# Kernel tuning notes

Measured on AMD Instinct MI355X. Metric: run time of the kernel, lower is better.

## Reference

```python
import jax, jax.numpy as jnp
import numpy as np

N = 50000   # nodes
E = 600000  # edges
D = 128     # node_features (EvolveGCNO in=out channels)
H = 128     # hidden_dim (final Linear out)


def setup_inputs() -> dict:
    key = jax.random.key(0)
    ks = jax.random.split(key, 9)
    stdv = 1.0 / np.sqrt(D)
    u = lambda k, shape: jax.random.uniform(k, shape, jnp.float32, -stdv, stdv)
    return {
        "x": jax.random.normal(ks[0], (N, D), jnp.float32),
        "edge_index": jax.random.randint(ks[1], (2, E), 0, N),
        "edge_weight": jax.random.uniform(ks[2], (E,), jnp.float32),
        "W0": u(ks[3], (D, D)),        # EvolveGCNO initial_weight (squeezed)
        "w_ih": u(ks[4], (3 * D, D)),  # GRU input weights (r|z|n)
        "w_hh": u(ks[5], (3 * D, D)),  # GRU hidden weights (r|z|n)
        "b_ih": u(ks[6], (3 * D,)),
        "b_hh": u(ks[7], (3 * D,)),
        "W_lin": u(ks[8], (H, D)),     # torch Linear weight [out, in]
        "b_lin": jnp.zeros((H,), jnp.float32),
    }


def _gru_step(x, h, w_ih, w_hh, b_ih, b_hh):
    # One torch.nn.GRU cell step; here x == h == W0 (weight evolution).
    gi = x @ w_ih.T + b_ih
    gh = h @ w_hh.T + b_hh
    i_r, i_z, i_n = jnp.split(gi, 3, axis=-1)
    h_r, h_z, h_n = jnp.split(gh, 3, axis=-1)
    r = jax.nn.sigmoid(i_r + h_r)
    z = jax.nn.sigmoid(i_z + h_z)
    n = jnp.tanh(i_n + r * h_n)
    return (1.0 - z) * n + z * h


def reference(x, edge_index, edge_weight, W0, w_ih, w_hh, b_ih, b_hh, W_lin, b_lin):
    # 1) Evolve the GCN weight with one GRU step (input = hidden = W0).
    W = _gru_step(W0, W0, w_ih, w_hh, b_ih, b_hh)  # [D, D]

    # 2) GCNConv_Fixed_W: add self-loops (weight 1), symmetric normalization.
    loops = jnp.arange(N)
    row = jnp.concatenate([edge_index[0], loops])  # source
    col = jnp.concatenate([edge_index[1], loops])  # target
    ew = jnp.concatenate([edge_weight, jnp.ones((N,), x.dtype)])
    deg = jax.ops.segment_sum(ew, col, num_segments=N)
    dinv = jnp.where(deg > 0, jax.lax.rsqrt(deg), 0.0)
    norm = dinv[row] * ew * dinv[col]  # [E+N]

    xw = x @ W                                        # [N, D]
    h = jax.ops.segment_sum(norm[:, None] * xw[row], col, num_segments=N)  # [N, D]

    # 3) ReLU + Linear
    h = jax.nn.relu(h)
    return h @ W_lin.T + b_lin  # [N, H]
```

## Files before the change

### kernel.cpp

```cpp
#include <hip/hip_runtime.h>
#include <hip/hip_bf16.h>

#define NN 50000
#define EE 600000
#define DD 128
#define CAP 48
#define CNT_SHIFT 25
#define SUM_MASK 0x1FFFFFFu

typedef __attribute__((ext_vector_type(8))) __bf16 bf16x8;
typedef __attribute__((ext_vector_type(8))) short short8;
typedef __attribute__((ext_vector_type(4))) float f32x4;

__device__ __forceinline__ unsigned short f2bf(float f) {
    union { float f; unsigned u; } c; c.f = f;
    unsigned r = (c.u + 0x7fffu + ((c.u >> 16) & 1u)) >> 16;
    return (unsigned short)r;
}
__device__ __forceinline__ float bflo(unsigned u) {
    union { unsigned u; float f; } c; c.u = u << 16; return c.f;
}
__device__ __forceinline__ float bfhi(unsigned u) {
    union { unsigned u; float f; } c; c.u = u & 0xffff0000u; return c.f;
}
__device__ __forceinline__ float degof(unsigned p) {
    return 1.0f + (float)(p & SUM_MASK) * (1.0f / 65536.0f);
}

__global__ __launch_bounds__(256) void init_kernel(
    unsigned* __restrict__ cnt32,
    const float* __restrict__ W0, const float* __restrict__ w_ih,
    const float* __restrict__ w_hh, const float* __restrict__ b_ih,
    const float* __restrict__ b_hh, unsigned short* __restrict__ Wbt,
    const float* __restrict__ x, short* __restrict__ xb)
{
    if (blockIdx.x >= 113) {
        int u = (blockIdx.x - 113) * 256 + threadIdx.x;
        if (u < NN * DD / 8) {
            const float4* p = (const float4*)x + (size_t)u * 2;
            float4 f0 = p[0], f1 = p[1];
            short8 v;
            v[0] = (short)f2bf(f0.x); v[1] = (short)f2bf(f0.y);
            v[2] = (short)f2bf(f0.z); v[3] = (short)f2bf(f0.w);
            v[4] = (short)f2bf(f1.x); v[5] = (short)f2bf(f1.y);
            v[6] = (short)f2bf(f1.z); v[7] = (short)f2bf(f1.w);
            *(short8*)(xb + (size_t)u * 8) = v;
        }
        return;
    }
    if (blockIdx.x < 49) {
        int i = blockIdx.x * 256 + threadIdx.x;
        if (i < 50176 * 4 / 16) ((uint4*)cnt32)[i] = make_uint4(0u, 0u, 0u, 0u);
        return;
    }
    int idx = (blockIdx.x - 49) * 256 + threadIdx.x;
    int i = idx >> 7, j = idx & 127;
    const float4* a  = (const float4*)(W0  + i * DD);
    const float4* pr = (const float4*)(w_ih + (j        ) * DD);
    const float4* pz = (const float4*)(w_ih + (j + 128  ) * DD);
    const float4* pn = (const float4*)(w_ih + (j + 256  ) * DD);
    const float4* qr = (const float4*)(w_hh + (j        ) * DD);
    const float4* qz = (const float4*)(w_hh + (j + 128  ) * DD);
    const float4* qn = (const float4*)(w_hh + (j + 256  ) * DD);
    float ir = 0.f, iz = 0.f, inn = 0.f, hr = 0.f, hz = 0.f, hn = 0.f;
    for (int d = 0; d < DD / 4; ++d) {
        float4 av = a[d];
        float4 t;
        t = pr[d]; ir  += av.x*t.x + av.y*t.y + av.z*t.z + av.w*t.w;
        t = pz[d]; iz  += av.x*t.x + av.y*t.y + av.z*t.z + av.w*t.w;
        t = pn[d]; inn += av.x*t.x + av.y*t.y + av.z*t.z + av.w*t.w;
        t = qr[d]; hr  += av.x*t.x + av.y*t.y + av.z*t.z + av.w*t.w;
        t = qz[d]; hz  += av.x*t.x + av.y*t.y + av.z*t.z + av.w*t.w;
        t = qn[d]; hn  += av.x*t.x + av.y*t.y + av.z*t.z + av.w*t.w;
    }
    ir += b_ih[j]; iz += b_ih[j + 128]; inn += b_ih[j + 256];
    hr += b_hh[j]; hz += b_hh[j + 128]; hn  += b_hh[j + 256];
    float r = 1.f / (1.f + expf(-(ir + hr)));
    float z = 1.f / (1.f + expf(-(iz + hz)));
    float n = tanhf(inn + r * hn);
    float w = (1.f - z) * n + z * W0[idx];
    Wbt[j * DD + i] = f2bf(w);
}

__global__ __launch_bounds__(256) void histfill_kernel(
    const int* __restrict__ row, const int* __restrict__ col,
    const float* __restrict__ ew,
    unsigned* __restrict__ cnt32, unsigned* __restrict__ edges)
{
    int e = blockIdx.x * 512 + threadIdx.x;
#pragma unroll
    for (int q = 0; q < 2; ++q, e += 256) {
        if (e < EE) {
            int c = col[e];
            unsigned wq = (unsigned)(ew[e] * 65536.0f);
            if (wq > 65535u) wq = 65535u;
            unsigned old = atomicAdd(&cnt32[c], (1u << CNT_SHIFT) | wq);
            unsigned oldcnt = old >> CNT_SHIFT;
            if (oldcnt < CAP)
                edges[(size_t)c * CAP + oldcnt] = (unsigned)row[e] | (wq << 16);
        }
    }
}

__global__ __launch_bounds__(256) void gather_kernel(
    const unsigned* __restrict__ edges, const unsigned* __restrict__ cnt32,
    const unsigned* __restrict__ xbu, unsigned* __restrict__ aggu)
{
    int wid  = threadIdx.x >> 6;
    int lane = threadIdx.x & 63;
    int base = (blockIdx.x * 4 + wid) * 2;
    if (base >= NN) return;
    bool hasB = (base + 1) < NN;

    unsigned pnA = cnt32[base];
    unsigned pnB = hasB ? cnt32[base + 1] : 0u;
    int nA = (int)(pnA >> CNT_SHIFT); if (nA > CAP) nA = CAP;
    int nB = hasB ? (int)(pnB >> CNT_SHIFT) : 0; if (nB > CAP) nB = CAP;
    const unsigned* ebA = edges + (size_t)base * CAP;
    const unsigned* ebB = edges + (size_t)(base + 1) * CAP;
    float sclA = rsqrtf(degof(pnA));
    float sclB = hasB ? rsqrtf(degof(pnB)) : 0.f;
    unsigned xsA = xbu[(size_t)base * 64 + lane];
    unsigned xsB = hasB ? xbu[(size_t)(base + 1) * 64 + lane] : 0u;
    float axA = sclA * bflo(xsA), ayA = sclA * bfhi(xsA);
    float axB = sclB * bflo(xsB), ayB = sclB * bfhi(xsB);

    int kA = 0, kB = 0;
    int nA4 = nA & ~3, nB4 = nB & ~3;
    while (kA < nA4 || kB < nB4) {
        if (kA < nA4) {
            uint4 rc = *(const uint4*)(ebA + kA);
            int s0 = (int)(rc.x & 0xFFFFu), s1 = (int)(rc.y & 0xFFFFu);
            int s2 = (int)(rc.z & 0xFFFFu), s3 = (int)(rc.w & 0xFFFFu);
            unsigned p0 = cnt32[s0], p1 = cnt32[s1], p2 = cnt32[s2], p3 = cnt32[s3];
            unsigned x0 = xbu[(size_t)s0 * 64 + lane];
            unsigned x1 = xbu[(size_t)s1 * 64 + lane];
            unsigned x2 = xbu[(size_t)s2 * 64 + lane];
            unsigned x3 = xbu[(size_t)s3 * 64 + lane];
            float v0 = (float)(rc.x >> 16) * (1.0f / 65536.0f) * rsqrtf(degof(p0));
            float v1 = (float)(rc.y >> 16) * (1.0f / 65536.0f) * rsqrtf(degof(p1));
            float v2 = (float)(rc.z >> 16) * (1.0f / 65536.0f) * rsqrtf(degof(p2));
            float v3 = (float)(rc.w >> 16) * (1.0f / 65536.0f) * rsqrtf(degof(p3));
            axA += v0 * bflo(x0) + v1 * bflo(x1) + v2 * bflo(x2) + v3 * bflo(x3);
            ayA += v0 * bfhi(x0) + v1 * bfhi(x1) + v2 * bfhi(x2) + v3 * bfhi(x3);
            kA += 4;
        }
        if (kB < nB4) {
            uint4 rc = *(const uint4*)(ebB + kB);
            int s0 = (int)(rc.x & 0xFFFFu), s1 = (int)(rc.y & 0xFFFFu);
            int s2 = (int)(rc.z & 0xFFFFu), s3 = (int)(rc.w & 0xFFFFu);
            unsigned p0 = cnt32[s0], p1 = cnt32[s1], p2 = cnt32[s2], p3 = cnt32[s3];
            unsigned x0 = xbu[(size_t)s0 * 64 + lane];
            unsigned x1 = xbu[(size_t)s1 * 64 + lane];
            unsigned x2 = xbu[(size_t)s2 * 64 + lane];
            unsigned x3 = xbu[(size_t)s3 * 64 + lane];
            float v0 = (float)(rc.x >> 16) * (1.0f / 65536.0f) * rsqrtf(degof(p0));
            float v1 = (float)(rc.y >> 16) * (1.0f / 65536.0f) * rsqrtf(degof(p1));
            float v2 = (float)(rc.z >> 16) * (1.0f / 65536.0f) * rsqrtf(degof(p2));
            float v3 = (float)(rc.w >> 16) * (1.0f / 65536.0f) * rsqrtf(degof(p3));
            axB += v0 * bflo(x0) + v1 * bflo(x1) + v2 * bflo(x2) + v3 * bflo(x3);
            ayB += v0 * bfhi(x0) + v1 * bfhi(x1) + v2 * bfhi(x2) + v3 * bfhi(x3);
            kB += 4;
        }
    }
    for (; kA < nA; ++kA) {
        unsigned r0 = ebA[kA];
        int s0 = (int)(r0 & 0xFFFFu);
        unsigned p0 = cnt32[s0];
        unsigned x0 = xbu[(size_t)s0 * 64 + lane];
        float v0 = (float)(r0 >> 16) * (1.0f / 65536.0f) * rsqrtf(degof(p0));
        axA += v0 * bflo(x0); ayA += v0 * bfhi(x0);
    }
    for (; kB < nB; ++kB) {
        unsigned r0 = ebB[kB];
        int s0 = (int)(r0 & 0xFFFFu);
        unsigned p0 = cnt32[s0];
        unsigned x0 = xbu[(size_t)s0 * 64 + lane];
        float v0 = (float)(r0 >> 16) * (1.0f / 65536.0f) * rsqrtf(degof(p0));
        axB += v0 * bflo(x0); ayB += v0 * bfhi(x0);
    }
    aggu[(size_t)base * 64 + lane] =
        (unsigned)f2bf(axA * sclA) | ((unsigned)f2bf(ayA * sclA) << 16);
    if (hasB)
        aggu[(size_t)(base + 1) * 64 + lane] =
            (unsigned)f2bf(axB * sclB) | ((unsigned)f2bf(ayB * sclB) << 16);
}

__global__ __launch_bounds__(256) void fused_gemm(
    const short* __restrict__ agg, const short* __restrict__ Wbt,
    const float* __restrict__ Wlin, const float* __restrict__ bias,
    float* __restrict__ out)
{
    __shared__ __align__(16) short Bs1[DD * DD];
    __shared__ __align__(16) short Bs2[DD * DD];
    __shared__ __align__(16) short As[64 * DD];
    const int t = threadIdx.x;
    const int i0 = blockIdx.x * 64;

    for (int u = t; u < 2048; u += 256) {
        int byte = u << 4;
        int brow = byte >> 8;
        *(short8*)((char*)Bs1 + (byte ^ ((brow & 7) << 4))) =
            *(const short8*)((const char*)Wbt + byte);
    }
    for (int u = t; u < 2048; u += 256) {
        int brow = u >> 4;
        int kc = (u & 15) << 3;
        const float4* p = (const float4*)(Wlin + brow * DD + kc);
        float4 f0 = p[0], f1 = p[1];
        short8 v;
        v[0] = (short)f2bf(f0.x); v[1] = (short)f2bf(f0.y);
        v[2] = (short)f2bf(f0.z); v[3] = (short)f2bf(f0.w);
        v[4] = (short)f2bf(f1.x); v[5] = (short)f2bf(f1.y);
        v[6] = (short)f2bf(f1.z); v[7] = (short)f2bf(f1.w);
        int byte = (brow << 8) + (kc << 1);
        *(short8*)((char*)Bs2 + (byte ^ ((brow & 7) << 4))) = v;
    }
    for (int u = t; u < 1024; u += 256) {
        int arow = u >> 4;
        int kc = (u & 15) << 3;
        int grow = i0 + arow;
        short8 v;
#pragma unroll
        for (int i = 0; i < 8; ++i) v[i] = 0;
        if (grow < NN)
            v = *(const short8*)(agg + (size_t)grow * DD + kc);
        int byte = (arow << 8) + (kc << 1);
        *(short8*)((char*)As + (byte ^ ((arow & 7) << 4))) = v;
    }
    __syncthreads();

    const int lane = t & 63, wv = t >> 6;
    const int c0 = lane & 15, g = lane >> 4;
    const int arow = wv * 16 + c0;
    f32x4 acc[8];
#pragma unroll
    for (int n = 0; n < 8; ++n) { acc[n][0] = acc[n][1] = acc[n][2] = acc[n][3] = 0.f; }

#pragma unroll
    for (int s = 0; s < 4; ++s) {
        int k0 = s * 32 + g * 8;
        int abyte = (arow << 8) + (k0 << 1);
        bf16x8 a = *(const bf16x8*)((const char*)As + (abyte ^ ((arow & 7) << 4)));
#pragma unroll
        for (int n = 0; n < 8; ++n) {
            int bcol = n * 16 + c0;
            int bbyte = (bcol << 8) + (k0 << 1);
            bf16x8 b = *(const bf16x8*)((const char*)Bs1 + (bbyte ^ ((bcol & 7) << 4)));
            acc[n] = __builtin_amdgcn_mfma_f32_16x16x32_bf16(a, b, acc[n], 0, 0, 0);
        }
    }
    __syncthreads();

#pragma unroll
    for (int n = 0; n < 8; ++n) {
        int ccol = n * 16 + c0;
#pragma unroll
        for (int r = 0; r < 4; ++r) {
            int hrow = wv * 16 + g * 4 + r;
            int byte = (hrow << 8) + (ccol << 1);
            *(unsigned short*)((char*)As + (byte ^ ((hrow & 7) << 4))) =
                f2bf(fmaxf(acc[n][r], 0.f));
        }
    }
    __syncthreads();

#pragma unroll
    for (int n = 0; n < 8; ++n) { acc[n][0] = acc[n][1] = acc[n][2] = acc[n][3] = 0.f; }

#pragma unroll
    for (int s = 0; s < 4; ++s) {
        int k0 = s * 32 + g * 8;
        int abyte = (arow << 8) + (k0 << 1);
        bf16x8 a = *(const bf16x8*)((const char*)As + (abyte ^ ((arow & 7) << 4)));
#pragma unroll
        for (int n = 0; n < 8; ++n) {
            int bcol = n * 16 + c0;
            int bbyte = (bcol << 8) + (k0 << 1);
            bf16x8 b = *(const bf16x8*)((const char*)Bs2 + (bbyte ^ ((bcol & 7) << 4)));
            acc[n] = __builtin_amdgcn_mfma_f32_16x16x32_bf16(a, b, acc[n], 0, 0, 0);
        }
    }

#pragma unroll
    for (int n = 0; n < 8; ++n) {
        int ccol = n * 16 + c0;
        float bb = bias[ccol];
#pragma unroll
        for (int r = 0; r < 4; ++r) {
            int grow = i0 + wv * 16 + g * 4 + r;
            if (grow < NN)
                out[(size_t)grow * DD + ccol] = acc[n][r] + bb;
        }
    }
}

extern "C" void kernel_launch(void* const* d_in, const int* in_sizes, int n_in,
                              void* d_out, int out_size, void* d_ws, size_t ws_size,
                              hipStream_t stream)
{
    const float* x    = (const float*)d_in[0];
    const int*   ei   = (const int*)d_in[1];
    const float* ew   = (const float*)d_in[2];
    const float* W0   = (const float*)d_in[3];
    const float* w_ih = (const float*)d_in[4];
    const float* w_hh = (const float*)d_in[5];
    const float* b_ih = (const float*)d_in[6];
    const float* b_hh = (const float*)d_in[7];
    const float* Wlin = (const float*)d_in[8];
    const float* blin = (const float*)d_in[9];
    float* out = (float*)d_out;

    const int* row = ei;
    const int* col = ei + EE;

    char* ws = (char*)d_ws;
    unsigned short* Wbt = (unsigned short*)ws;
    unsigned* cnt32 = (unsigned*)(ws + 32768);
    short* xb   = (short*)(ws + 233472);
    short* agg  = (short*)(ws + 13033472);
    unsigned* edges = (unsigned*)(ws + 25833472);

    init_kernel<<<3238, 256, 0, stream>>>(cnt32, W0, w_ih, w_hh, b_ih, b_hh, Wbt, x, xb);

    histfill_kernel<<<(EE + 511) / 512, 256, 0, stream>>>(row, col, ew, cnt32, edges);

    gather_kernel<<<(NN + 7) / 8, 256, 0, stream>>>(
        edges, cnt32, (const unsigned*)xb, (unsigned*)agg);

    fused_gemm<<<(NN + 63) / 64, 256, 0, stream>>>(
        agg, (const short*)Wbt, Wlin, blin, out);
}
```

Baseline: 125.6 us.

## Move x bf16 conversion into histfill kernel and precompute bf16 W_lin once

The fp32-to-bf16 conversion of x moves out of the init kernel and into the histogram/fill kernel as extra blocks, so the init kernel becomes tiny and the conversion runs alongside the atomic edge binning. W_lin is converted to bf16 once in init instead of in each of the ~782 GEMM blocks, so each GEMM block now only copies it into LDS. The histfill blocks also go from two edges per thread to one. In exchange there is an extra 32 KB workspace buffer and shifted workspace offsets.

Result: no change. 125.6 us (-0.0%).

```diff
diff --git a/kernel.cpp b/kernel.cpp
--- a/kernel.cpp
+++ b/kernel.cpp
@@ -8,6 +8,9 @@
 #define CNT_SHIFT 25
 #define SUM_MASK 0x1FFFFFFu
 
+#define HF_BLOCKS ((EE + 255) / 256)
+#define XC_BLOCKS (NN * DD / 8 / 256)
+
 typedef __attribute__((ext_vector_type(8))) __bf16 bf16x8;
 typedef __attribute__((ext_vector_type(8))) short short8;
 typedef __attribute__((ext_vector_type(4))) float f32x4;
@@ -32,25 +35,16 @@
     const float* __restrict__ W0, const float* __restrict__ w_ih,
     const float* __restrict__ w_hh, const float* __restrict__ b_ih,
     const float* __restrict__ b_hh, unsigned short* __restrict__ Wbt,
-    const float* __restrict__ x, short* __restrict__ xb)
-{
-    if (blockIdx.x >= 113) {
-        int u = (blockIdx.x - 113) * 256 + threadIdx.x;
-        if (u < NN * DD / 8) {
-            const float4* p = (const float4*)x + (size_t)u * 2;
-            float4 f0 = p[0], f1 = p[1];
-            short8 v;
-            v[0] = (short)f2bf(f0.x); v[1] = (short)f2bf(f0.y);
-            v[2] = (short)f2bf(f0.z); v[3] = (short)f2bf(f0.w);
-            v[4] = (short)f2bf(f1.x); v[5] = (short)f2bf(f1.y);
-            v[6] = (short)f2bf(f1.z); v[7] = (short)f2bf(f1.w);
-            *(short8*)(xb + (size_t)u * 8) = v;
-        }
-        return;
-    }
+    const float* __restrict__ Wlin, unsigned short* __restrict__ Wlbt)
+{
     if (blockIdx.x < 49) {
         int i = blockIdx.x * 256 + threadIdx.x;
         if (i < 50176 * 4 / 16) ((uint4*)cnt32)[i] = make_uint4(0u, 0u, 0u, 0u);
+        return;
+    }
+    if (blockIdx.x >= 113) {
+        int idx = (blockIdx.x - 113) * 256 + threadIdx.x;
+        Wlbt[idx] = f2bf(Wlin[idx]);
         return;
     }
     int idx = (blockIdx.x - 49) * 256 + threadIdx.x;
@@ -82,14 +76,14 @@
     Wbt[j * DD + i] = f2bf(w);
 }
 
-__global__ __launch_bounds__(256) void histfill_kernel(
+__global__ __launch_bounds__(256) void hf_conv_kernel(
     const int* __restrict__ row, const int* __restrict__ col,
     const float* __restrict__ ew,
-    unsigned* __restrict__ cnt32, unsigned* __restrict__ edges)
-{
-    int e = blockIdx.x * 512 + threadIdx.x;
-#pragma unroll
-    for (int q = 0; q < 2; ++q, e += 256) {
+    unsigned* __restrict__ cnt32, unsigned* __restrict__ edges,
+    const float* __restrict__ x, short* __restrict__ xb)
+{
+    if (blockIdx.x < HF_BLOCKS) {
+        int e = blockIdx.x * 256 + threadIdx.x;
         if (e < EE) {
             int c = col[e];
             unsigned wq = (unsigned)(ew[e] * 65536.0f);
@@ -99,7 +93,17 @@
             if (oldcnt < CAP)
                 edges[(size_t)c * CAP + oldcnt] = (unsigned)row[e] | (wq << 16);
         }
-    }
+        return;
+    }
+    int u = (blockIdx.x - HF_BLOCKS) * 256 + threadIdx.x;
+    const float4* p = (const float4*)x + (size_t)u * 2;
+    float4 f0 = p[0], f1 = p[1];
+    short8 v;
+    v[0] = (short)f2bf(f0.x); v[1] = (short)f2bf(f0.y);
+    v[2] = (short)f2bf(f0.z); v[3] = (short)f2bf(f0.w);
+    v[4] = (short)f2bf(f1.x); v[5] = (short)f2bf(f1.y);
+    v[6] = (short)f2bf(f1.z); v[7] = (short)f2bf(f1.w);
+    *(short8*)(xb + (size_t)u * 8) = v;
 }
 
 __global__ __launch_bounds__(256) void gather_kernel(
@@ -188,7 +192,7 @@
 
 __global__ __launch_bounds__(256) void fused_gemm(
     const short* __restrict__ agg, const short* __restrict__ Wbt,
-    const float* __restrict__ Wlin, const float* __restrict__ bias,
+    const short* __restrict__ Wlbt, const float* __restrict__ bias,
     float* __restrict__ out)
 {
     __shared__ __align__(16) short Bs1[DD * DD];
@@ -200,21 +204,9 @@
     for (int u = t; u < 2048; u += 256) {
         int byte = u << 4;
         int brow = byte >> 8;
-        *(short8*)((char*)Bs1 + (byte ^ ((brow & 7) << 4))) =
-            *(const short8*)((const char*)Wbt + byte);
-    }
-    for (int u = t; u < 2048; u += 256) {
-        int brow = u >> 4;
-        int kc = (u & 15) << 3;
-        const float4* p = (const float4*)(Wlin + brow * DD + kc);
-        float4 f0 = p[0], f1 = p[1];
-        short8 v;
-        v[0] = (short)f2bf(f0.x); v[1] = (short)f2bf(f0.y);
-        v[2] = (short)f2bf(f0.z); v[3] = (short)f2bf(f0.w);
-        v[4] = (short)f2bf(f1.x); v[5] = (short)f2bf(f1.y);
-        v[6] = (short)f2bf(f1.z); v[7] = (short)f2bf(f1.w);
-        int byte = (brow << 8) + (kc << 1);
-        *(short8*)((char*)Bs2 + (byte ^ ((brow & 7) << 4))) = v;
+        int sw = byte ^ ((brow & 7) << 4);
+        *(short8*)((char*)Bs1 + sw) = *(const short8*)((const char*)Wbt + byte);
+        *(short8*)((char*)Bs2 + sw) = *(const short8*)((const char*)Wlbt + byte);
     }
     for (int u = t; u < 1024; u += 256) {
         int arow = u >> 4;
@@ -315,19 +307,22 @@
     const int* col = ei + EE;
 
     char* ws = (char*)d_ws;
-    unsigned short* Wbt = (unsigned short*)ws;
-    unsigned* cnt32 = (unsigned*)(ws + 32768);
-    short* xb   = (short*)(ws + 233472);
-    short* agg  = (short*)(ws + 13033472);
-    unsigned* edges = (unsigned*)(ws + 25833472);
-
-    init_kernel<<<3238, 256, 0, stream>>>(cnt32, W0, w_ih, w_hh, b_ih, b_hh, Wbt, x, xb);
-
-    histfill_kernel<<<(EE + 511) / 512, 256, 0, stream>>>(row, col, ew, cnt32, edges);
+    unsigned short* Wbt  = (unsigned short*)ws;
+    unsigned short* Wlbt = (unsigned short*)(ws + 32768);
+    unsigned* cnt32 = (unsigned*)(ws + 65536);
+    short* xb   = (short*)(ws + 266240);
+    short* agg  = (short*)(ws + 13066240);
+    unsigned* edges = (unsigned*)(ws + 25866240);
+
+    init_kernel<<<177, 256, 0, stream>>>(cnt32, W0, w_ih, w_hh, b_ih, b_hh,
+                                         Wbt, Wlin, Wlbt);
+
+    hf_conv_kernel<<<HF_BLOCKS + XC_BLOCKS, 256, 0, stream>>>(
+        row, col, ew, cnt32, edges, x, xb);
 
     gather_kernel<<<(NN + 7) / 8, 256, 0, stream>>>(
         edges, cnt32, (const unsigned*)xb, (unsigned*)agg);
 
     fused_gemm<<<(NN + 63) / 64, 256, 0, stream>>>(
-        agg, (const short*)Wbt, Wlin, blin, out);
-}
+        agg, (const short*)Wbt, (const short*)Wlbt, blin, out);
+}
```
